# Optimization experiments

Measured on AMD Instinct MI355X. Metric: run time of the kernel, lower is better.

The kernel has to match this reference:

```python
import jax, jax.numpy as jnp
import numpy as np

DEPTH_REF = jnp.array([28.01, 16.32], dtype=jnp.float32)
DIM_REF = jnp.array([[3.88, 1.63, 1.53], [0.84, 1.76, 0.66], [1.78, 1.52, 1.78]], dtype=jnp.float32)
TOPK = 50
DET_THRESHOLD = 0.25
PI = 3.14159265358979


def nms_hm(heat, kernel=3):
    # 3x3 max-pool NMS: keep peaks, zero everything else
    pad = (kernel - 1) // 2
    hmax = jax.lax.reduce_window(heat, -jnp.inf, jax.lax.max,
                                 (1, 1, kernel, kernel), (1, 1, 1, 1),
                                 [(0, 0), (0, 0), (pad, pad), (pad, pad)])
    return jnp.where(hmax == heat, heat, 0.0)


def select_topk(heat, K):
    B, C, H, W = heat.shape
    scores_all, inds_all = jax.lax.top_k(heat.reshape(B, C, H * W), K)  # [B,C,K]
    ys_all = (inds_all // W).astype(jnp.float32)
    xs_all = (inds_all % W).astype(jnp.float32)
    scores, inds = jax.lax.top_k(scores_all.reshape(B, C * K), K)       # [B,K] over classes
    clses = (inds // K).astype(jnp.float32)
    topk_inds = jnp.take_along_axis(inds_all.reshape(B, C * K), inds, axis=1)
    ys = jnp.take_along_axis(ys_all.reshape(B, C * K), inds, axis=1)
    xs = jnp.take_along_axis(xs_all.reshape(B, C * K), inds, axis=1)
    return scores, topk_inds, clses, ys, xs


def select_point_of_interest(index, feature_maps):
    B, Cf, H, W = feature_maps.shape
    fm = feature_maps.transpose(0, 2, 3, 1).reshape(B, H * W, Cf)
    return jnp.take_along_axis(fm, index[:, :, None], axis=1)  # [B,K,Cf]


def encode_box3d(rotys, dims, locs):
    # dims = (l, h, w); corner signs reproduce SMOKE's gather pattern
    N = rotys.shape[0]
    c, s = jnp.cos(rotys), jnp.sin(rotys)
    z, o = jnp.zeros_like(c), jnp.ones_like(c)
    ry = jnp.stack([c, z, s, z, o, z, -s, z, c], axis=1).reshape(N, 3, 3)
    sx = jnp.array([-0.5, 0.5, 0.5, 0.5, 0.5, -0.5, -0.5, -0.5], dtype=dims.dtype)
    sy = jnp.array([-1., -1., 0., 0., -1., -1., 0., 0.], dtype=dims.dtype)
    sz = jnp.array([-0.5, -0.5, -0.5, 0.5, 0.5, 0.5, 0.5, -0.5], dtype=dims.dtype)
    corners = jnp.stack([dims[:, 0:1] * sx, dims[:, 1:2] * sy, dims[:, 2:3] * sz], axis=1)  # [N,3,8]
    return jnp.einsum('nij,njk->nik', ry, corners) + locs[:, :, None]


def setup_inputs() -> dict:
    key = jax.random.key(0)
    k1, k2 = jax.random.split(key)
    B, C, H, W = 32, 3, 192, 640
    IMG_W, IMG_H = 4 * W, 4 * H
    pred_heatmap = jax.random.uniform(k1, (B, C, H, W), dtype=jnp.float32)
    pred_regression = jax.random.normal(k2, (B, 8, H, W), dtype=jnp.float32) * 0.5
    # affine image->heatmap (scale 1/4), invertible
    tm = jnp.array([[0.25, 0., 0.], [0., 0.25, 0.], [0., 0., 1.]], dtype=jnp.float32)
    trans_mat = jnp.tile(tm[None], (B, 1, 1))
    Kc = jnp.array([[721.5, 0., IMG_W / 2.], [0., 721.5, IMG_H / 2.], [0., 0., 1.]], dtype=jnp.float32)
    K_mat = jnp.tile(Kc[None], (B, 1, 1))
    img_size = jnp.tile(jnp.array([[IMG_W, IMG_H]], dtype=jnp.float32), (B, 1))
    return {"pred_heatmap": pred_heatmap, "pred_regression": pred_regression,
            "trans_mat": trans_mat, "K_mat": K_mat, "img_size": img_size}


def reference(pred_heatmap, pred_regression, trans_mat, K_mat, img_size):
    B = pred_heatmap.shape[0]
    heat = nms_hm(pred_heatmap)
    scores, inds, clses, ys, xs = select_topk(heat, TOPK)
    reg = select_point_of_interest(inds, pred_regression).reshape(-1, 8)  # [B*K,8]

    points = jnp.stack([xs.reshape(-1), ys.reshape(-1)], axis=1)          # heatmap coords
    depth_off, proj_off = reg[:, 0], reg[:, 1:3]
    dim_off, ori = reg[:, 3:6], reg[:, 6:8]
    cls_idx = clses.reshape(-1).astype(jnp.int32)

    obj_id = jnp.repeat(jnp.arange(B), TOPK)
    tm_inv = jnp.linalg.inv(trans_mat)[obj_id]   # [N,3,3]
    K_inv = jnp.linalg.inv(K_mat)[obj_id]

    # decode location: heatmap -> image -> camera frame
    proj = points + proj_off
    proj_ext = jnp.concatenate([proj, jnp.ones_like(proj[:, :1])], axis=1)
    proj_img = jnp.einsum('nij,nj->ni', tm_inv, proj_ext)                 # image-plane homog coords
    depths = depth_off * DEPTH_REF[1] + DEPTH_REF[0]
    locs = jnp.einsum('nij,nj->ni', K_inv, proj_img * depths[:, None])

    dims = jnp.exp(dim_off) * DIM_REF[cls_idx]                            # (l,h,w)
    locs = locs.at[:, 1].add(dims[:, 1] / 2)

    # decode orientation
    eps = 1e-7
    rays = jnp.arctan(locs[:, 0] / (locs[:, 2] + eps))
    alphas = jnp.arctan(ori[:, 0] / (ori[:, 1] + eps))
    alphas = jnp.where(ori[:, 1] >= 0, alphas - PI / 2, alphas + PI / 2)
    rotys = alphas + rays
    wrap = lambda a: jnp.where(a > PI, a - 2 * PI, jnp.where(a < -PI, a + 2 * PI, a))
    rotys, alphas = wrap(rotys), wrap(alphas)

    # encode 2D boxes from projected 3D corners
    corners = encode_box3d(rotys, dims, locs)                             # [N,3,8]
    proj2 = jnp.einsum('nij,njk->nik', K_mat[obj_id], corners)
    xy = proj2[:, :2] / proj2[:, 2:3]
    Wi, Hi = img_size[obj_id, 0], img_size[obj_id, 1]
    xmins = jnp.clip(xy[:, 0].min(axis=1), 0.0, Wi)
    ymins = jnp.clip(xy[:, 1].min(axis=1), 0.0, Hi)
    xmaxs = jnp.clip(xy[:, 0].max(axis=1), 0.0, Wi)
    ymaxs = jnp.clip(xy[:, 1].max(axis=1), 0.0, Hi)
    box2d = jnp.stack([xmins, ymins, xmaxs, ymaxs], axis=1)

    dims_rolled = jnp.roll(dims, -1, axis=1)                              # (h,w,l)
    result = jnp.concatenate([
        cls_idx.astype(jnp.float32)[:, None], alphas[:, None], box2d,
        dims_rolled, locs, rotys[:, None], scores.reshape(-1, 1)], axis=1)  # [B*K,14]
    keep = result[:, -1] > DET_THRESHOLD
    return jnp.where(keep[:, None], result, 0.0)
```

## Files before the change

### kernel.cpp

```cpp
#include <hip/hip_runtime.h>
#include <math.h>

#define Hd 192
#define Wd 640
#define HWp (Hd * Wd)
#define NCLS 3
#define KTOP 50
#define NB 32
#define NPL (NB * NCLS)
#define GPR 160
#define GPP (HWp / 4)
#define SPR 40
#define SEGBLK 30
#define SEGCAP 64
#define CAP 2048
#define RBK 256
#define PI_F 3.14159265358979f

#define OFF_COUNTS 0
#define OFF_SEGKEY 16384
#define OFF_PSC 0x200000
#define OFF_PPI 0x206000

__device__ inline float fmax3(float a, float b, float c) {
  return fmaxf(fmaxf(a, b), c);
}

template <typename F>
__device__ inline void peaks_in_group(const float* __restrict__ p, int g, F&& f) {
  const int y = g / GPR;
  const int x0 = (g - y * GPR) * 4;
  const float* rm = p + y * Wd + x0;
  const float4 mq = *(const float4*)rm;
  const float ml = (x0 > 0) ? rm[-1] : -INFINITY;
  const float mr = (x0 + 4 < Wd) ? rm[4] : -INFINITY;
  float4 tq; float tl, tr;
  if (y > 0) {
    const float* rt = rm - Wd;
    tq = *(const float4*)rt;
    tl = (x0 > 0) ? rt[-1] : -INFINITY;
    tr = (x0 + 4 < Wd) ? rt[4] : -INFINITY;
  } else {
    tq.x = tq.y = tq.z = tq.w = -INFINITY; tl = -INFINITY; tr = -INFINITY;
  }
  float4 bq; float bl, br;
  if (y < Hd - 1) {
    const float* rb = rm + Wd;
    bq = *(const float4*)rb;
    bl = (x0 > 0) ? rb[-1] : -INFINITY;
    br = (x0 + 4 < Wd) ? rb[4] : -INFINITY;
  } else {
    bq.x = bq.y = bq.z = bq.w = -INFINITY; bl = -INFINITY; br = -INFINITY;
  }
  const float c0 = fmax3(tl, ml, bl);
  const float c1 = fmax3(tq.x, mq.x, bq.x);
  const float c2 = fmax3(tq.y, mq.y, bq.y);
  const float c3 = fmax3(tq.z, mq.z, bq.z);
  const float c4 = fmax3(tq.w, mq.w, bq.w);
  const float c5 = fmax3(tr, mr, br);
  const int base = y * Wd + x0;
  if (mq.x == fmax3(c0, c1, c2)) f(__float_as_uint(mq.x), base + 0);
  if (mq.y == fmax3(c1, c2, c3)) f(__float_as_uint(mq.y), base + 1);
  if (mq.z == fmax3(c2, c3, c4)) f(__float_as_uint(mq.z), base + 2);
  if (mq.w == fmax3(c3, c4, c5)) f(__float_as_uint(mq.w), base + 3);
}

template <typename F>
__device__ inline void for_each_peak_plane(const float* __restrict__ p, int tid,
                                           int nth, F&& f) {
  for (int g = tid; g < GPP; g += nth) peaks_in_group(p, g, f);
}

__device__ inline unsigned long long mk_key(unsigned int bits, int idx) {
  return ((unsigned long long)bits << 32) | (unsigned int)~idx;
}

__device__ inline int bucket_of(unsigned int bits) {
  const unsigned int base = __float_as_uint(0.995f);
  if (bits <= base) return 0;
  unsigned int d = (bits - base) >> 9;
  return d > 255u ? 255 : (int)d;
}

struct Row16 {
  float4 q0, q1, q2, q3;
  float l, r;
};

__device__ inline Row16 load_row16(const float* __restrict__ rp, int x0, bool valid) {
  Row16 o;
  if (valid) {
    o.q0 = *(const float4*)(rp);
    o.q1 = *(const float4*)(rp + 4);
    o.q2 = *(const float4*)(rp + 8);
    o.q3 = *(const float4*)(rp + 12);
    o.l = (x0 > 0) ? rp[-1] : -INFINITY;
    o.r = (x0 + 16 < Wd) ? rp[16] : -INFINITY;
  } else {
    o.q0.x = o.q0.y = o.q0.z = o.q0.w = -INFINITY;
    o.q1 = o.q0; o.q2 = o.q0; o.q3 = o.q0;
    o.l = -INFINITY; o.r = -INFINITY;
  }
  return o;
}

__device__ inline float4 max3v(const float4 a, const float4 b, const float4 c) {
  float4 o;
  o.x = fmax3(a.x, b.x, c.x);
  o.y = fmax3(a.y, b.y, c.y);
  o.z = fmax3(a.z, b.z, c.z);
  o.w = fmax3(a.w, b.w, c.w);
  return o;
}

__device__ inline void inv3(const float* m, float* o) {
  float a = m[0], b = m[1], c = m[2];
  float d = m[3], e = m[4], f = m[5];
  float g = m[6], h = m[7], i = m[8];
  float A = e * i - f * h;
  float B = -(d * i - f * g);
  float C = d * h - e * g;
  float det = a * A + b * B + c * C;
  float id = 1.0f / det;
  o[0] = A * id;            o[1] = -(b * i - c * h) * id; o[2] = (b * f - c * e) * id;
  o[3] = B * id;            o[4] = (a * i - c * g) * id;  o[5] = -(a * f - c * d) * id;
  o[6] = C * id;            o[7] = -(a * h - b * g) * id; o[8] = (a * e - b * d) * id;
}

__device__ inline float wrap_pi(float a) {
  if (a > PI_F) return a - 2.0f * PI_F;
  if (a < -PI_F) return a + 2.0f * PI_F;
  return a;
}

__constant__ float DIM_REF_C[9] = {3.88f, 1.63f, 1.53f,
                                   0.84f, 1.76f, 0.66f,
                                   1.78f, 1.52f, 1.78f};

__global__ __launch_bounds__(256) void scan_kernel(
    const float* __restrict__ heat,
    int* __restrict__ counts,
    unsigned long long* __restrict__ segkey) {
  const int blk = blockIdx.x;
  const int plane = blk / SEGBLK;
  const int sub = blk - plane * SEGBLK;
  __shared__ unsigned long long s_k[SEGCAP];
  __shared__ int s_n;
  if (threadIdx.x == 0) s_n = 0;
  __syncthreads();

  const int strip = sub * 256 + threadIdx.x;
  const int y = strip / SPR;
  const int x0 = (strip - y * SPR) * 16;
  const float* pm = heat + (size_t)plane * HWp + y * Wd + x0;

  const Row16 m = load_row16(pm, x0, true);
  const Row16 t = load_row16(pm - Wd, x0, y > 0);
  const Row16 b = load_row16(pm + Wd, x0, y < Hd - 1);

  const float cl = fmax3(t.l, m.l, b.l);
  const float cr = fmax3(t.r, m.r, b.r);
  const float4 c0 = max3v(t.q0, m.q0, b.q0);
  const float4 c1 = max3v(t.q1, m.q1, b.q1);
  const float4 c2 = max3v(t.q2, m.q2, b.q2);
  const float4 c3 = max3v(t.q3, m.q3, b.q3);

  const float TH = 0.995f;
  const int base = y * Wd + x0;
#define EMIT(V, W0, W1, W2, J)                                         \
  if ((V) >= TH && (V) == fmax3((W0), (W1), (W2))) {                   \
    int slot = atomicAdd(&s_n, 1);                                     \
    if (slot < SEGCAP) s_k[slot] = mk_key(__float_as_uint(V), base + (J)); \
  }
  EMIT(m.q0.x, cl,   c0.x, c0.y, 0)
  EMIT(m.q0.y, c0.x, c0.y, c0.z, 1)
  EMIT(m.q0.z, c0.y, c0.z, c0.w, 2)
  EMIT(m.q0.w, c0.z, c0.w, c1.x, 3)
  EMIT(m.q1.x, c0.w, c1.x, c1.y, 4)
  EMIT(m.q1.y, c1.x, c1.y, c1.z, 5)
  EMIT(m.q1.z, c1.y, c1.z, c1.w, 6)
  EMIT(m.q1.w, c1.z, c1.w, c2.x, 7)
  EMIT(m.q2.x, c1.w, c2.x, c2.y, 8)
  EMIT(m.q2.y, c2.x, c2.y, c2.z, 9)
  EMIT(m.q2.z, c2.y, c2.z, c2.w, 10)
  EMIT(m.q2.w, c2.z, c2.w, c3.x, 11)
  EMIT(m.q3.x, c2.w, c3.x, c3.y, 12)
  EMIT(m.q3.y, c3.x, c3.y, c3.z, 13)
  EMIT(m.q3.z, c3.y, c3.z, c3.w, 14)
  EMIT(m.q3.w, c3.z, c3.w, cr,   15)
#undef EMIT

  __syncthreads();
  const int n = s_n;
  if (threadIdx.x == 0) counts[blk] = n;
  const int nn = n < SEGCAP ? n : SEGCAP;
  if (threadIdx.x < nn)
    segkey[(size_t)blk * SEGCAP + threadIdx.x] = s_k[threadIdx.x];
}

__global__ __launch_bounds__(256) void rank_kernel(
    const float* __restrict__ heat,
    const int* __restrict__ counts,
    const unsigned long long* __restrict__ segkey,
    float* __restrict__ plane_sc,
    int* __restrict__ plane_pi) {
  const int plane = blockIdx.x;
  const int tid = threadIdx.x;

  __shared__ unsigned long long s_key[CAP];
  __shared__ unsigned long long c_key[CAP];
  __shared__ int s_off[SEGBLK + 1];
  __shared__ int cnt[RBK], suf[RBK], cur[RBK];
  __shared__ int s_flag, s_M, s_fast;
  __shared__ int s_fbB, s_fbAbove, s_fbT, s_fbCnt;

  if (tid == 0) { s_flag = 0; s_off[0] = 0; }
  __syncthreads();
  if (tid < SEGBLK) {
    int nv = counts[plane * SEGBLK + tid];
    if (nv > SEGCAP) { atomicOr(&s_flag, 1); nv = SEGCAP; }
    s_off[tid + 1] = nv;
  }
  __syncthreads();
  if (tid == 0) {
    int acc = 0;
    for (int i = 1; i <= SEGBLK; ++i) { acc += s_off[i]; s_off[i] = acc; }
    s_M = acc;
    s_fast = (s_flag == 0) && (acc >= KTOP) && (acc <= CAP);
  }
  __syncthreads();

  if (s_fast) {
    const unsigned long long* pk = segkey + (size_t)plane * SEGBLK * SEGCAP;
    for (int i = tid; i < SEGBLK * SEGCAP; i += 256) {
      const int sg = i >> 6;
      const int j = i & (SEGCAP - 1);
      const int o = s_off[sg];
      const int nsg = s_off[sg + 1] - o;
      if (j < nsg) s_key[o + j] = pk[i];
    }
    __syncthreads();
  } else {
    const float* hp = heat + (size_t)plane * HWp;
    unsigned int* fb_hist = (unsigned int*)c_key;
    for (int i = tid; i < 1024; i += 256) fb_hist[i] = 0;
    __syncthreads();
    for_each_peak_plane(hp, tid, 256, [&](unsigned int bits, int idx) {
      unsigned int bkt = bits >> 20; if (bkt > 1023u) bkt = 1023u;
      atomicAdd(&fb_hist[bkt], 1u);
    });
    __syncthreads();
    if (tid == 0) {
      int acc = 0, Bs = -1;
      for (int bkt = 1023; bkt >= 0; --bkt) {
        int cc = (int)fb_hist[bkt];
        if (acc + cc >= KTOP) { Bs = bkt; s_fbAbove = acc; break; }
        acc += cc;
      }
      s_fbB = Bs;
      if (Bs < 0) s_fbAbove = acc;
    }
    __syncthreads();
    const int Bs = s_fbB;
    unsigned int T;
    if (Bs < 0) {
      T = 0;
    } else {
      for (int i = tid; i < 1024; i += 256) fb_hist[i] = 0;
      __syncthreads();
      for_each_peak_plane(hp, tid, 256, [&](unsigned int bits, int idx) {
        unsigned int bkt = bits >> 20; if (bkt > 1023u) bkt = 1023u;
        if ((int)bkt == Bs) atomicAdd(&fb_hist[(bits >> 10) & 1023], 1u);
      });
      __syncthreads();
      if (tid == 0) {
        int acc = s_fbAbove, Ss = 0;
        for (int sb = 1023; sb >= 0; --sb) {
          int cc = (int)fb_hist[sb];
          if (acc + cc >= KTOP) { Ss = sb; break; }
          acc += cc;
        }
        s_fbT = (int)(((unsigned int)Bs << 20) | ((unsigned int)Ss << 10));
      }
      __syncthreads();
      T = (unsigned int)s_fbT;
    }
    if (tid == 0) s_fbCnt = 0;
    __syncthreads();
    for_each_peak_plane(hp, tid, 256, [&](unsigned int bits, int idx) {
      if (bits >= T) {
        int slot = atomicAdd(&s_fbCnt, 1);
        if (slot < CAP) s_key[slot] = mk_key(bits, idx);
      }
    });
    __syncthreads();
    if (tid == 0) s_M = s_fbCnt < CAP ? s_fbCnt : CAP;
    __syncthreads();
  }
  const int M = s_M;

  cnt[tid] = 0;
  cur[tid] = 0;
  __syncthreads();
  for (int i = tid; i < M; i += 256)
    atomicAdd(&cnt[bucket_of((unsigned int)(s_key[i] >> 32))], 1);
  __syncthreads();
  suf[tid] = cnt[tid];
  __syncthreads();
#pragma unroll
  for (int d = 1; d < RBK; d <<= 1) {
    const int v = (tid + d < RBK) ? suf[tid + d] : 0;
    __syncthreads();
    suf[tid] += v;
    __syncthreads();
  }
  {
    const int excl = suf[tid] - cnt[tid];
    __syncthreads();
    suf[tid] = excl;
  }
  __syncthreads();
  for (int i = tid; i < M; i += 256) {
    const unsigned long long k = s_key[i];
    const int bq = bucket_of((unsigned int)(k >> 32));
    const int slot = suf[bq] + atomicAdd(&cur[bq], 1);
    c_key[slot] = k;
  }
  __syncthreads();
  float* psc = plane_sc + plane * 64;
  int* ppi = plane_pi + plane * 64;
  for (int i = tid; i < M; i += 256) {
    const unsigned long long k = c_key[i];
    const int bq = bucket_of((unsigned int)(k >> 32));
    const int st = suf[bq];
    const int nb = cnt[bq];
    int rank = st;
    for (int tt = st; tt < st + nb; ++tt) rank += (c_key[tt] > k);
    if (rank < KTOP) {
      psc[rank] = __uint_as_float((unsigned int)(k >> 32));
      ppi[rank] = (int)~((unsigned int)k);
    }
  }
  for (int s2 = M + tid; s2 < KTOP; s2 += 256) {
    psc[s2] = 0.0f;
    ppi[s2] = 0;
  }
}

__global__ __launch_bounds__(256) void decode_kernel(
    const float* __restrict__ plane_sc,
    const int* __restrict__ plane_pi,
    const float* __restrict__ regr,
    const float* __restrict__ trans_mat,
    const float* __restrict__ K_mat,
    const float* __restrict__ img_size,
    float* __restrict__ out) {
  const int b = blockIdx.x;
  const int tid = threadIdx.x;

  __shared__ float d_sc[NCLS * KTOP];
  __shared__ int d_pi[NCLS * KTOP];
  __shared__ int sel[KTOP];

  if (tid < NCLS * KTOP) {
    const int c = tid / KTOP;
    const int k2 = tid - c * KTOP;
    d_sc[tid] = plane_sc[(b * NCLS + c) * 64 + k2];
    d_pi[tid] = plane_pi[(b * NCLS + c) * 64 + k2];
  }
  __syncthreads();

  if (tid < NCLS * KTOP) {
    const float v = d_sc[tid];
    int rank = 0;
    for (int j = 0; j < NCLS * KTOP; ++j) {
      const float w = d_sc[j];
      rank += (w > v) || (w == v && j < tid);
    }
    if (rank < KTOP) sel[rank] = tid;
  }
  __syncthreads();

  if (tid < KTOP) {
    const int i = sel[tid];
    const int cls = i / KTOP;
    const float score = d_sc[i];
    const int ind = d_pi[i];
    const float ys = (float)(ind / Wd);
    const float xs = (float)(ind - (ind / Wd) * Wd);

    const float* rb = regr + (size_t)b * 8 * HWp + ind;
    const float r0 = rb[0 * HWp], r1 = rb[1 * HWp], r2 = rb[2 * HWp], r3 = rb[3 * HWp];
    const float r4 = rb[4 * HWp], r5 = rb[5 * HWp], r6 = rb[6 * HWp], r7 = rb[7 * HWp];

    float tm[9], km[9], tmi[9], kmi[9];
#pragma unroll
    for (int q = 0; q < 9; ++q) { tm[q] = trans_mat[b * 9 + q]; km[q] = K_mat[b * 9 + q]; }
    inv3(tm, tmi);
    inv3(km, kmi);

    const float px = xs + r1, py = ys + r2;
    const float gx = tmi[0] * px + tmi[1] * py + tmi[2];
    const float gy = tmi[3] * px + tmi[4] * py + tmi[5];
    const float gz = tmi[6] * px + tmi[7] * py + tmi[8];
    const float depth = r0 * 16.32f + 28.01f;
    const float qx = gx * depth, qy = gy * depth, qz = gz * depth;
    const float lx = kmi[0] * qx + kmi[1] * qy + kmi[2] * qz;
    float ly = kmi[3] * qx + kmi[4] * qy + kmi[5] * qz;
    const float lz = kmi[6] * qx + kmi[7] * qy + kmi[8] * qz;

    const float d0 = expf(r3) * DIM_REF_C[cls * 3 + 0];
    const float d1 = expf(r4) * DIM_REF_C[cls * 3 + 1];
    const float d2 = expf(r5) * DIM_REF_C[cls * 3 + 2];
    ly += d1 * 0.5f;

    const float ray = atanf(lx / (lz + 1e-7f));
    float alpha = atanf(r6 / (r7 + 1e-7f));
    alpha += (r7 >= 0.0f) ? -PI_F * 0.5f : PI_F * 0.5f;
    const float roty = wrap_pi(alpha + ray);
    alpha = wrap_pi(alpha);

    const float SX[8] = {-0.5f, 0.5f, 0.5f, 0.5f, 0.5f, -0.5f, -0.5f, -0.5f};
    const float SY[8] = {-1.0f, -1.0f, 0.0f, 0.0f, -1.0f, -1.0f, 0.0f, 0.0f};
    const float SZ[8] = {-0.5f, -0.5f, -0.5f, 0.5f, 0.5f, 0.5f, 0.5f, -0.5f};
    const float cr = cosf(roty), sr = sinf(roty);
    float minx = INFINITY, maxx = -INFINITY, miny = INFINITY, maxy = -INFINITY;
#pragma unroll
    for (int j = 0; j < 8; ++j) {
      const float ax = d0 * SX[j], ay = d1 * SY[j], az = d2 * SZ[j];
      const float cx = cr * ax + sr * az + lx;
      const float cy = ay + ly;
      const float cz = -sr * ax + cr * az + lz;
      const float ppx = km[0] * cx + km[1] * cy + km[2] * cz;
      const float ppy = km[3] * cx + km[4] * cy + km[5] * cz;
      const float ppz = km[6] * cx + km[7] * cy + km[8] * cz;
      const float X = ppx / ppz, Y = ppy / ppz;
      minx = fminf(minx, X); maxx = fmaxf(maxx, X);
      miny = fminf(miny, Y); maxy = fmaxf(maxy, Y);
    }
    const float Wi = img_size[b * 2 + 0], Hi = img_size[b * 2 + 1];
    const float xmin = fminf(fmaxf(minx, 0.0f), Wi);
    const float ymin = fminf(fmaxf(miny, 0.0f), Hi);
    const float xmax = fminf(fmaxf(maxx, 0.0f), Wi);
    const float ymax = fminf(fmaxf(maxy, 0.0f), Hi);

    float* o = out + (size_t)(b * KTOP + tid) * 14;
    if (score > 0.25f) {
      o[0] = (float)cls; o[1] = alpha;
      o[2] = xmin; o[3] = ymin; o[4] = xmax; o[5] = ymax;
      o[6] = d1; o[7] = d2; o[8] = d0;
      o[9] = lx; o[10] = ly; o[11] = lz;
      o[12] = roty; o[13] = score;
    } else {
#pragma unroll
      for (int q = 0; q < 14; ++q) o[q] = 0.0f;
    }
  }
}


extern "C" void kernel_launch(void* const* d_in, const int* in_sizes, int n_in,
                              void* d_out, int out_size, void* d_ws, size_t ws_size,
                              hipStream_t stream) {
  const float* heat = (const float*)d_in[0];
  const float* regr = (const float*)d_in[1];
  const float* tmat = (const float*)d_in[2];
  const float* kmat = (const float*)d_in[3];
  const float* isz = (const float*)d_in[4];

  char* ws = (char*)d_ws;
  int* counts = (int*)(ws + OFF_COUNTS);
  unsigned long long* segkey = (unsigned long long*)(ws + OFF_SEGKEY);
  float* plane_sc = (float*)(ws + OFF_PSC);
  int* plane_pi = (int*)(ws + OFF_PPI);

  scan_kernel<<<NPL * SEGBLK, 256, 0, stream>>>(heat, counts, segkey);
  rank_kernel<<<NPL, 256, 0, stream>>>(heat, counts, segkey,
                                       plane_sc, plane_pi);
  decode_kernel<<<NB, 256, 0, stream>>>(plane_sc, plane_pi,
                                        regr, tmat, kmat, isz,
                                        (float*)d_out);
}
```

Baseline: 211.5 us.

## Fuse peak scan with per-segment top-K and merge segments in decode

Merges the scan and rank kernels into one kernel, so each of 576 blocks scans a sixth of a heatmap plane and computes its local top-50, with an in-block histogram threshold fallback when candidates overflow. The decode kernel then merges the six segment lists per class using 64-bit packed keys and a bucket prefilter, and falls back to a full-plane scan only when a class has fewer than K candidates. This drops one kernel launch and the global round trip of segment keys. In exchange each block does more serial work and uses more shared memory, and the decode kernel grows larger.

```diff
diff --git a/kernel.cpp b/kernel.cpp
--- a/kernel.cpp
+++ b/kernel.cpp
@@ -8,78 +8,42 @@
 #define KTOP 50
 #define NB 32
 #define NPL (NB * NCLS)
+#define SPR 40
+#define TSTR (Hd * SPR)
+#define NSUB 6
+#define SSTR (TSTR / NSUB)
+#define CAPS 512
+#define CAP 2048
+#define RBK 256
 #define GPR 160
 #define GPP (HWp / 4)
-#define SPR 40
-#define SEGBLK 30
-#define SEGCAP 64
-#define CAP 2048
-#define RBK 256
+#define NMERGE (NCLS * NSUB * KTOP)
+#define TH_F 0.995f
 #define PI_F 3.14159265358979f
 
-#define OFF_COUNTS 0
-#define OFF_SEGKEY 16384
-#define OFF_PSC 0x200000
-#define OFF_PPI 0x206000
+#define OFF_SSC 0
+#define OFF_SPI 0x40000
+#define OFF_SCNT 0x80000
 
 __device__ inline float fmax3(float a, float b, float c) {
   return fmaxf(fmaxf(a, b), c);
 }
 
-template <typename F>
-__device__ inline void peaks_in_group(const float* __restrict__ p, int g, F&& f) {
-  const int y = g / GPR;
-  const int x0 = (g - y * GPR) * 4;
-  const float* rm = p + y * Wd + x0;
-  const float4 mq = *(const float4*)rm;
-  const float ml = (x0 > 0) ? rm[-1] : -INFINITY;
-  const float mr = (x0 + 4 < Wd) ? rm[4] : -INFINITY;
-  float4 tq; float tl, tr;
-  if (y > 0) {
-    const float* rt = rm - Wd;
-    tq = *(const float4*)rt;
-    tl = (x0 > 0) ? rt[-1] : -INFINITY;
-    tr = (x0 + 4 < Wd) ? rt[4] : -INFINITY;
-  } else {
-    tq.x = tq.y = tq.z = tq.w = -INFINITY; tl = -INFINITY; tr = -INFINITY;
-  }
-  float4 bq; float bl, br;
-  if (y < Hd - 1) {
-    const float* rb = rm + Wd;
-    bq = *(const float4*)rb;
-    bl = (x0 > 0) ? rb[-1] : -INFINITY;
-    br = (x0 + 4 < Wd) ? rb[4] : -INFINITY;
-  } else {
-    bq.x = bq.y = bq.z = bq.w = -INFINITY; bl = -INFINITY; br = -INFINITY;
-  }
-  const float c0 = fmax3(tl, ml, bl);
-  const float c1 = fmax3(tq.x, mq.x, bq.x);
-  const float c2 = fmax3(tq.y, mq.y, bq.y);
-  const float c3 = fmax3(tq.z, mq.z, bq.z);
-  const float c4 = fmax3(tq.w, mq.w, bq.w);
-  const float c5 = fmax3(tr, mr, br);
-  const int base = y * Wd + x0;
-  if (mq.x == fmax3(c0, c1, c2)) f(__float_as_uint(mq.x), base + 0);
-  if (mq.y == fmax3(c1, c2, c3)) f(__float_as_uint(mq.y), base + 1);
-  if (mq.z == fmax3(c2, c3, c4)) f(__float_as_uint(mq.z), base + 2);
-  if (mq.w == fmax3(c3, c4, c5)) f(__float_as_uint(mq.w), base + 3);
-}
-
-template <typename F>
-__device__ inline void for_each_peak_plane(const float* __restrict__ p, int tid,
-                                           int nth, F&& f) {
-  for (int g = tid; g < GPP; g += nth) peaks_in_group(p, g, f);
-}
-
 __device__ inline unsigned long long mk_key(unsigned int bits, int idx) {
   return ((unsigned long long)bits << 32) | (unsigned int)~idx;
 }
 
 __device__ inline int bucket_of(unsigned int bits) {
-  const unsigned int base = __float_as_uint(0.995f);
+  const unsigned int base = __float_as_uint(TH_F);
   if (bits <= base) return 0;
   unsigned int d = (bits - base) >> 9;
   return d > 255u ? 255 : (int)d;
+}
+
+__device__ inline unsigned long long mk_key19(unsigned int bits, int cls, int idx) {
+  return ((unsigned long long)bits << 19) |
+         ((unsigned long long)(2 - cls) << 17) |
+         (unsigned long long)((idx ^ 0x1FFFF) & 0x1FFFF);
 }
 
 struct Row16 {
@@ -113,65 +77,24 @@
   return o;
 }
 
-__device__ inline void inv3(const float* m, float* o) {
-  float a = m[0], b = m[1], c = m[2];
-  float d = m[3], e = m[4], f = m[5];
-  float g = m[6], h = m[7], i = m[8];
-  float A = e * i - f * h;
-  float B = -(d * i - f * g);
-  float C = d * h - e * g;
-  float det = a * A + b * B + c * C;
-  float id = 1.0f / det;
-  o[0] = A * id;            o[1] = -(b * i - c * h) * id; o[2] = (b * f - c * e) * id;
-  o[3] = B * id;            o[4] = (a * i - c * g) * id;  o[5] = -(a * f - c * d) * id;
-  o[6] = C * id;            o[7] = -(a * h - b * g) * id; o[8] = (a * e - b * d) * id;
-}
-
-__device__ inline float wrap_pi(float a) {
-  if (a > PI_F) return a - 2.0f * PI_F;
-  if (a < -PI_F) return a + 2.0f * PI_F;
-  return a;
-}
-
-__constant__ float DIM_REF_C[9] = {3.88f, 1.63f, 1.53f,
-                                   0.84f, 1.76f, 0.66f,
-                                   1.78f, 1.52f, 1.78f};
-
-__global__ __launch_bounds__(256) void scan_kernel(
-    const float* __restrict__ heat,
-    int* __restrict__ counts,
-    unsigned long long* __restrict__ segkey) {
-  const int blk = blockIdx.x;
-  const int plane = blk / SEGBLK;
-  const int sub = blk - plane * SEGBLK;
-  __shared__ unsigned long long s_k[SEGCAP];
-  __shared__ int s_n;
-  if (threadIdx.x == 0) s_n = 0;
-  __syncthreads();
-
-  const int strip = sub * 256 + threadIdx.x;
+template <typename F>
+__device__ inline void strip_peaks(const float* __restrict__ hp, int strip, F&& f) {
   const int y = strip / SPR;
   const int x0 = (strip - y * SPR) * 16;
-  const float* pm = heat + (size_t)plane * HWp + y * Wd + x0;
-
+  const float* pm = hp + y * Wd + x0;
   const Row16 m = load_row16(pm, x0, true);
   const Row16 t = load_row16(pm - Wd, x0, y > 0);
   const Row16 b = load_row16(pm + Wd, x0, y < Hd - 1);
-
   const float cl = fmax3(t.l, m.l, b.l);
   const float cr = fmax3(t.r, m.r, b.r);
   const float4 c0 = max3v(t.q0, m.q0, b.q0);
   const float4 c1 = max3v(t.q1, m.q1, b.q1);
   const float4 c2 = max3v(t.q2, m.q2, b.q2);
   const float4 c3 = max3v(t.q3, m.q3, b.q3);
-
-  const float TH = 0.995f;
   const int base = y * Wd + x0;
-#define EMIT(V, W0, W1, W2, J)                                         \
-  if ((V) >= TH && (V) == fmax3((W0), (W1), (W2))) {                   \
-    int slot = atomicAdd(&s_n, 1);                                     \
-    if (slot < SEGCAP) s_k[slot] = mk_key(__float_as_uint(V), base + (J)); \
-  }
+#define EMIT(V, W0, W1, W2, J)                                       \
+  if ((V) >= TH_F && (V) == fmax3((W0), (W1), (W2)))                 \
+    f(__float_as_uint(V), base + (J));
   EMIT(m.q0.x, cl,   c0.x, c0.y, 0)
   EMIT(m.q0.y, c0.x, c0.y, c0.z, 1)
   EMIT(m.q0.z, c0.y, c0.z, c0.w, 2)
@@ -189,120 +112,169 @@
   EMIT(m.q3.z, c3.y, c3.z, c3.w, 14)
   EMIT(m.q3.w, c3.z, c3.w, cr,   15)
 #undef EMIT
-
-  __syncthreads();
-  const int n = s_n;
-  if (threadIdx.x == 0) counts[blk] = n;
-  const int nn = n < SEGCAP ? n : SEGCAP;
-  if (threadIdx.x < nn)
-    segkey[(size_t)blk * SEGCAP + threadIdx.x] = s_k[threadIdx.x];
-}
-
-__global__ __launch_bounds__(256) void rank_kernel(
+}
+
+template <typename F>
+__device__ inline void peaks_in_group(const float* __restrict__ p, int g, F&& f) {
+  const int y = g / GPR;
+  const int x0 = (g - y * GPR) * 4;
+  const float* rm = p + y * Wd + x0;
+  const float4 mq = *(const float4*)rm;
+  const float ml = (x0 > 0) ? rm[-1] : -INFINITY;
+  const float mr = (x0 + 4 < Wd) ? rm[4] : -INFINITY;
+  float4 tq; float tl, tr;
+  if (y > 0) {
+    const float* rt = rm - Wd;
+    tq = *(const float4*)rt;
+    tl = (x0 > 0) ? rt[-1] : -INFINITY;
+    tr = (x0 + 4 < Wd) ? rt[4] : -INFINITY;
+  } else {
+    tq.x = tq.y = tq.z = tq.w = -INFINITY; tl = -INFINITY; tr = -INFINITY;
+  }
+  float4 bq; float bl, br;
+  if (y < Hd - 1) {
+    const float* rb = rm + Wd;
+    bq = *(const float4*)rb;
+    bl = (x0 > 0) ? rb[-1] : -INFINITY;
+    br = (x0 + 4 < Wd) ? rb[4] : -INFINITY;
+  } else {
+    bq.x = bq.y = bq.z = bq.w = -INFINITY; bl = -INFINITY; br = -INFINITY;
+  }
+  const float c0 = fmax3(tl, ml, bl);
+  const float c1 = fmax3(tq.x, mq.x, bq.x);
+  const float c2 = fmax3(tq.y, mq.y, bq.y);
+  const float c3 = fmax3(tq.z, mq.z, bq.z);
+  const float c4 = fmax3(tq.w, mq.w, bq.w);
+  const float c5 = fmax3(tr, mr, br);
+  const int base = y * Wd + x0;
+  if (mq.x == fmax3(c0, c1, c2)) f(__float_as_uint(mq.x), base + 0);
+  if (mq.y == fmax3(c1, c2, c3)) f(__float_as_uint(mq.y), base + 1);
+  if (mq.z == fmax3(c2, c3, c4)) f(__float_as_uint(mq.z), base + 2);
+  if (mq.w == fmax3(c3, c4, c5)) f(__float_as_uint(mq.w), base + 3);
+}
+
+template <typename F>
+__device__ inline void for_each_peak_plane(const float* __restrict__ p, int tid,
+                                           int nth, F&& f) {
+  for (int g = tid; g < GPP; g += nth) peaks_in_group(p, g, f);
+}
+
+__device__ inline void inv3(const float* m, float* o) {
+  float a = m[0], b = m[1], c = m[2];
+  float d = m[3], e = m[4], f = m[5];
+  float g = m[6], h = m[7], i = m[8];
+  float A = e * i - f * h;
+  float B = -(d * i - f * g);
+  float C = d * h - e * g;
+  float det = a * A + b * B + c * C;
+  float id = 1.0f / det;
+  o[0] = A * id;            o[1] = -(b * i - c * h) * id; o[2] = (b * f - c * e) * id;
+  o[3] = B * id;            o[4] = (a * i - c * g) * id;  o[5] = -(a * f - c * d) * id;
+  o[6] = C * id;            o[7] = -(a * h - b * g) * id; o[8] = (a * e - b * d) * id;
+}
+
+__device__ inline float wrap_pi(float a) {
+  if (a > PI_F) return a - 2.0f * PI_F;
+  if (a < -PI_F) return a + 2.0f * PI_F;
+  return a;
+}
+
+__constant__ float DIM_REF_C[9] = {3.88f, 1.63f, 1.53f,
+                                   0.84f, 1.76f, 0.66f,
+                                   1.78f, 1.52f, 1.78f};
+
+__global__ __launch_bounds__(256) void scanrank_kernel(
     const float* __restrict__ heat,
-    const int* __restrict__ counts,
-    const unsigned long long* __restrict__ segkey,
-    float* __restrict__ plane_sc,
-    int* __restrict__ plane_pi) {
-  const int plane = blockIdx.x;
+    float* __restrict__ ssc,
+    int* __restrict__ spi,
+    int* __restrict__ scnt) {
+  const int blk = blockIdx.x;
   const int tid = threadIdx.x;
-
-  __shared__ unsigned long long s_key[CAP];
-  __shared__ unsigned long long c_key[CAP];
-  __shared__ int s_off[SEGBLK + 1];
+  const int plane = blk / NSUB;
+  const int sub = blk - plane * NSUB;
+  const float* hp = heat + (size_t)plane * HWp;
+  const int sbase = sub * SSTR;
+
+  __shared__ unsigned long long s_key[CAPS];
+  __shared__ unsigned long long c_key[CAPS];
   __shared__ int cnt[RBK], suf[RBK], cur[RBK];
-  __shared__ int s_flag, s_M, s_fast;
-  __shared__ int s_fbB, s_fbAbove, s_fbT, s_fbCnt;
-
-  if (tid == 0) { s_flag = 0; s_off[0] = 0; }
-  __syncthreads();
-  if (tid < SEGBLK) {
-    int nv = counts[plane * SEGBLK + tid];
-    if (nv > SEGCAP) { atomicOr(&s_flag, 1); nv = SEGCAP; }
-    s_off[tid + 1] = nv;
-  }
-  __syncthreads();
-  if (tid == 0) {
-    int acc = 0;
-    for (int i = 1; i <= SEGBLK; ++i) { acc += s_off[i]; s_off[i] = acc; }
-    s_M = acc;
-    s_fast = (s_flag == 0) && (acc >= KTOP) && (acc <= CAP);
-  }
-  __syncthreads();
-
-  if (s_fast) {
-    const unsigned long long* pk = segkey + (size_t)plane * SEGBLK * SEGCAP;
-    for (int i = tid; i < SEGBLK * SEGCAP; i += 256) {
-      const int sg = i >> 6;
-      const int j = i & (SEGCAP - 1);
-      const int o = s_off[sg];
-      const int nsg = s_off[sg + 1] - o;
-      if (j < nsg) s_key[o + j] = pk[i];
-    }
-    __syncthreads();
-  } else {
-    const float* hp = heat + (size_t)plane * HWp;
-    unsigned int* fb_hist = (unsigned int*)c_key;
-    for (int i = tid; i < 1024; i += 256) fb_hist[i] = 0;
-    __syncthreads();
-    for_each_peak_plane(hp, tid, 256, [&](unsigned int bits, int idx) {
-      unsigned int bkt = bits >> 20; if (bkt > 1023u) bkt = 1023u;
-      atomicAdd(&fb_hist[bkt], 1u);
+  __shared__ int s_n, s_B, s_above, s_T;
+
+  if (tid == 0) s_n = 0;
+  __syncthreads();
+
+  for (int it = 0; it < SSTR / 256; ++it) {
+    const int strip = sbase + it * 256 + tid;
+    strip_peaks(hp, strip, [&](unsigned int bits, int idx) {
+      int slot = atomicAdd(&s_n, 1);
+      if (slot < CAPS) s_key[slot] = mk_key(bits, idx);
     });
+  }
+  __syncthreads();
+  int n = s_n;
+
+  if (n > CAPS) {
+    unsigned int* hist = (unsigned int*)c_key;
+    const unsigned int THB = __float_as_uint(TH_F);
+    for (int i = tid; i < 1024; i += 256) hist[i] = 0;
+    __syncthreads();
+    for (int it = 0; it < SSTR / 256; ++it) {
+      const int strip = sbase + it * 256 + tid;
+      strip_peaks(hp, strip, [&](unsigned int bits, int idx) {
+        atomicAdd(&hist[(bits - THB) >> 7], 1u);
+      });
+    }
     __syncthreads();
     if (tid == 0) {
-      int acc = 0, Bs = -1;
-      for (int bkt = 1023; bkt >= 0; --bkt) {
-        int cc = (int)fb_hist[bkt];
-        if (acc + cc >= KTOP) { Bs = bkt; s_fbAbove = acc; break; }
+      int acc = 0, res = 0, above = 0;
+      for (int q = 655; q >= 0; --q) {
+        int cc = (int)hist[q];
+        if (acc + cc >= KTOP) { res = q; above = acc; break; }
         acc += cc;
       }
-      s_fbB = Bs;
-      if (Bs < 0) s_fbAbove = acc;
-    }
-    __syncthreads();
-    const int Bs = s_fbB;
-    unsigned int T;
-    if (Bs < 0) {
-      T = 0;
-    } else {
-      for (int i = tid; i < 1024; i += 256) fb_hist[i] = 0;
-      __syncthreads();
-      for_each_peak_plane(hp, tid, 256, [&](unsigned int bits, int idx) {
-        unsigned int bkt = bits >> 20; if (bkt > 1023u) bkt = 1023u;
-        if ((int)bkt == Bs) atomicAdd(&fb_hist[(bits >> 10) & 1023], 1u);
+      s_B = res; s_above = above;
+    }
+    __syncthreads();
+    const int Bc = s_B;
+    for (int i = tid; i < 1024; i += 256) hist[i] = 0;
+    __syncthreads();
+    for (int it = 0; it < SSTR / 256; ++it) {
+      const int strip = sbase + it * 256 + tid;
+      strip_peaks(hp, strip, [&](unsigned int bits, int idx) {
+        if ((int)((bits - THB) >> 7) == Bc)
+          atomicAdd(&hist[(bits - THB) & 127], 1u);
       });
-      __syncthreads();
-      if (tid == 0) {
-        int acc = s_fbAbove, Ss = 0;
-        for (int sb = 1023; sb >= 0; --sb) {
-          int cc = (int)fb_hist[sb];
-          if (acc + cc >= KTOP) { Ss = sb; break; }
-          acc += cc;
+    }
+    __syncthreads();
+    if (tid == 0) {
+      int acc = s_above, S = 0;
+      for (int sb = 127; sb >= 0; --sb) {
+        int cc = (int)hist[sb];
+        if (acc + cc >= KTOP) { S = sb; break; }
+        acc += cc;
+      }
+      s_T = (int)(THB + ((unsigned int)Bc << 7) + (unsigned int)S);
+      s_n = 0;
+    }
+    __syncthreads();
+    const unsigned int T = (unsigned int)s_T;
+    for (int it = 0; it < SSTR / 256; ++it) {
+      const int strip = sbase + it * 256 + tid;
+      strip_peaks(hp, strip, [&](unsigned int bits, int idx) {
+        if (bits >= T) {
+          int slot = atomicAdd(&s_n, 1);
+          if (slot < CAPS) s_key[slot] = mk_key(bits, idx);
         }
-        s_fbT = (int)(((unsigned int)Bs << 20) | ((unsigned int)Ss << 10));
-      }
-      __syncthreads();
-      T = (unsigned int)s_fbT;
-    }
-    if (tid == 0) s_fbCnt = 0;
-    __syncthreads();
-    for_each_peak_plane(hp, tid, 256, [&](unsigned int bits, int idx) {
-      if (bits >= T) {
-        int slot = atomicAdd(&s_fbCnt, 1);
-        if (slot < CAP) s_key[slot] = mk_key(bits, idx);
-      }
-    });
-    __syncthreads();
-    if (tid == 0) s_M = s_fbCnt < CAP ? s_fbCnt : CAP;
-    __syncthreads();
-  }
-  const int M = s_M;
+      });
+    }
+    __syncthreads();
+    n = s_n < CAPS ? s_n : CAPS;
+  }
 
   cnt[tid] = 0;
   cur[tid] = 0;
   __syncthreads();
-  for (int i = tid; i < M; i += 256)
+  for (int i = tid; i < n; i += 256)
     atomicAdd(&cnt[bucket_of((unsigned int)(s_key[i] >> 32))], 1);
   __syncthreads();
   suf[tid] = cnt[tid];
@@ -320,16 +292,16 @@
     suf[tid] = excl;
   }
   __syncthreads();
-  for (int i = tid; i < M; i += 256) {
+  for (int i = tid; i < n; i += 256) {
     const unsigned long long k = s_key[i];
     const int bq = bucket_of((unsigned int)(k >> 32));
     const int slot = suf[bq] + atomicAdd(&cur[bq], 1);
     c_key[slot] = k;
   }
   __syncthreads();
-  float* psc = plane_sc + plane * 64;
-  int* ppi = plane_pi + plane * 64;
-  for (int i = tid; i < M; i += 256) {
+  float* psc = ssc + blk * 64;
+  int* ppi = spi + blk * 64;
+  for (int i = tid; i < n; i += 256) {
     const unsigned long long k = c_key[i];
     const int bq = bucket_of((unsigned int)(k >> 32));
     const int st = suf[bq];
@@ -341,15 +313,18 @@
       ppi[rank] = (int)~((unsigned int)k);
     }
   }
-  for (int s2 = M + tid; s2 < KTOP; s2 += 256) {
+  for (int s2 = n + tid; s2 < KTOP; s2 += 256) {
     psc[s2] = 0.0f;
     ppi[s2] = 0;
   }
+  if (tid == 0) scnt[blk] = n;
 }
 
 __global__ __launch_bounds__(256) void decode_kernel(
-    const float* __restrict__ plane_sc,
-    const int* __restrict__ plane_pi,
+    const float* __restrict__ heat,
+    const float* __restrict__ ssc,
+    const int* __restrict__ spi,
+    const int* __restrict__ scnt,
     const float* __restrict__ regr,
     const float* __restrict__ trans_mat,
     const float* __restrict__ K_mat,
@@ -358,34 +333,190 @@
   const int b = blockIdx.x;
   const int tid = threadIdx.x;
 
-  __shared__ float d_sc[NCLS * KTOP];
-  __shared__ int d_pi[NCLS * KTOP];
+  __shared__ unsigned long long d_keys[NMERGE];
+  __shared__ unsigned long long f_keys[NCLS * KTOP];
+  __shared__ unsigned char d_in[NMERGE];
+  __shared__ int hb[NCLS][RBK];
+  __shared__ int s_bq[NCLS];
+  __shared__ int s_ct[NCLS];
   __shared__ int sel[KTOP];
+  __shared__ unsigned long long s_key[CAP];
+  __shared__ unsigned long long c_key[CAP];
+  __shared__ int cnt[RBK], suf[RBK], cur[RBK];
+  __shared__ int s_fbB, s_fbAbove, s_fbT, s_fbCnt;
+
+  if (tid < NCLS) {
+    int t = 0;
+    for (int s = 0; s < NSUB; ++s) t += scnt[(b * NCLS + tid) * NSUB + s];
+    s_ct[tid] = t;
+  }
+  __syncthreads();
+
+  for (int i = tid; i < NMERGE; i += 256) {
+    const int c = i / (NSUB * KTOP);
+    const int rem = i - c * (NSUB * KTOP);
+    const int s = rem / KTOP;
+    const int k2 = rem - s * KTOP;
+    const int sb = (b * NCLS + c) * NSUB + s;
+    const float v = ssc[sb * 64 + k2];
+    const int idx = spi[sb * 64 + k2];
+    d_keys[i] = mk_key19(__float_as_uint(v), c, idx);
+  }
+  __syncthreads();
+
+  for (int c = 0; c < NCLS; ++c) {
+    if (s_ct[c] < KTOP) {
+      const float* hp = heat + (size_t)(b * NCLS + c) * HWp;
+      unsigned int* fb_hist = (unsigned int*)c_key;
+      for (int i = tid; i < 1024; i += 256) fb_hist[i] = 0;
+      __syncthreads();
+      for_each_peak_plane(hp, tid, 256, [&](unsigned int bits, int idx) {
+        unsigned int bkt = bits >> 20; if (bkt > 1023u) bkt = 1023u;
+        atomicAdd(&fb_hist[bkt], 1u);
+      });
+      __syncthreads();
+      if (tid == 0) {
+        int acc = 0, Bs = -1;
+        for (int bkt = 1023; bkt >= 0; --bkt) {
+          int cc = (int)fb_hist[bkt];
+          if (acc + cc >= KTOP) { Bs = bkt; s_fbAbove = acc; break; }
+          acc += cc;
+        }
+        s_fbB = Bs;
+        if (Bs < 0) s_fbAbove = acc;
+      }
+      __syncthreads();
+      const int Bs = s_fbB;
+      unsigned int T;
+      if (Bs < 0) {
+        T = 0;
+      } else {
+        for (int i = tid; i < 1024; i += 256) fb_hist[i] = 0;
+        __syncthreads();
+        for_each_peak_plane(hp, tid, 256, [&](unsigned int bits, int idx) {
+          unsigned int bkt = bits >> 20; if (bkt > 1023u) bkt = 1023u;
+          if ((int)bkt == Bs) atomicAdd(&fb_hist[(bits >> 10) & 1023], 1u);
+        });
+        __syncthreads();
+        if (tid == 0) {
+          int acc = s_fbAbove, Ss = 0;
+          for (int sb = 1023; sb >= 0; --sb) {
+            int cc = (int)fb_hist[sb];
+            if (acc + cc >= KTOP) { Ss = sb; break; }
+            acc += cc;
+          }
+          s_fbT = (int)(((unsigned int)Bs << 20) | ((unsigned int)Ss << 10));
+        }
+        __syncthreads();
+        T = (unsigned int)s_fbT;
+      }
+      if (tid == 0) s_fbCnt = 0;
+      __syncthreads();
+      for_each_peak_plane(hp, tid, 256, [&](unsigned int bits, int idx) {
+        if (bits >= T) {
+          int slot = atomicAdd(&s_fbCnt, 1);
+          if (slot < CAP) s_key[slot] = mk_key(bits, idx);
+        }
+      });
+      __syncthreads();
+      const int M = s_fbCnt < CAP ? s_fbCnt : CAP;
+      cnt[tid] = 0; cur[tid] = 0;
+      __syncthreads();
+      for (int i = tid; i < M; i += 256)
+        atomicAdd(&cnt[bucket_of((unsigned int)(s_key[i] >> 32))], 1);
+      __syncthreads();
+      suf[tid] = cnt[tid];
+      __syncthreads();
+#pragma unroll
+      for (int d = 1; d < RBK; d <<= 1) {
+        const int v = (tid + d < RBK) ? suf[tid + d] : 0;
+        __syncthreads();
+        suf[tid] += v;
+        __syncthreads();
+      }
+      {
+        const int excl = suf[tid] - cnt[tid];
+        __syncthreads();
+        suf[tid] = excl;
+      }
+      __syncthreads();
+      for (int i = tid; i < M; i += 256) {
+        const unsigned long long k = s_key[i];
+        const int bq = bucket_of((unsigned int)(k >> 32));
+        const int slot = suf[bq] + atomicAdd(&cur[bq], 1);
+        c_key[slot] = k;
+      }
+      __syncthreads();
+      for (int i = tid; i < NMERGE / NCLS; i += 256)
+        d_keys[c * (NSUB * KTOP) + i] = mk_key19(0u, c, 0);
+      __syncthreads();
+      for (int i = tid; i < M; i += 256) {
+        const unsigned long long k = c_key[i];
+        const int bq = bucket_of((unsigned int)(k >> 32));
+        const int st = suf[bq];
+        const int nb = cnt[bq];
+        int rank = st;
+        for (int tt = st; tt < st + nb; ++tt) rank += (c_key[tt] > k);
+        if (rank < KTOP)
+          d_keys[c * (NSUB * KTOP) + rank] =
+              mk_key19((unsigned int)(k >> 32), c, (int)~((unsigned int)k));
+      }
+      __syncthreads();
+    }
+  }
+
+  for (int i = tid; i < NCLS * RBK; i += 256) ((int*)hb)[i] = 0;
+  __syncthreads();
+  for (int i = tid; i < NMERGE; i += 256) {
+    const int c = i / (NSUB * KTOP);
+    atomicAdd(&hb[c][bucket_of((unsigned int)(d_keys[i] >> 19))], 1);
+  }
+  __syncthreads();
+  if (tid < NCLS) {
+    int acc = 0, res = 0;
+    for (int q = RBK - 1; q >= 0; --q) {
+      acc += hb[tid][q];
+      if (acc >= KTOP) { res = q; break; }
+    }
+    s_bq[tid] = res;
+  }
+  __syncthreads();
+  for (int i = tid; i < NMERGE; i += 256) {
+    const int c = i / (NSUB * KTOP);
+    d_in[i] = bucket_of((unsigned int)(d_keys[i] >> 19)) >= s_bq[c];
+  }
+  __syncthreads();
+  for (int i = tid; i < NMERGE; i += 256) {
+    if (!d_in[i]) continue;
+    const int c = i / (NSUB * KTOP);
+    const int lo = c * (NSUB * KTOP), hi = lo + (NSUB * KTOP);
+    const unsigned long long k = d_keys[i];
+    int rank = 0;
+    for (int j = lo; j < hi; ++j) {
+      if (!d_in[j]) continue;
+      const unsigned long long w = d_keys[j];
+      rank += (w > k) || (w == k && j < i);
+    }
+    if (rank < KTOP) f_keys[c * KTOP + rank] = k;
+  }
+  __syncthreads();
 
   if (tid < NCLS * KTOP) {
-    const int c = tid / KTOP;
-    const int k2 = tid - c * KTOP;
-    d_sc[tid] = plane_sc[(b * NCLS + c) * 64 + k2];
-    d_pi[tid] = plane_pi[(b * NCLS + c) * 64 + k2];
-  }
-  __syncthreads();
-
-  if (tid < NCLS * KTOP) {
-    const float v = d_sc[tid];
+    const unsigned long long k = f_keys[tid];
     int rank = 0;
     for (int j = 0; j < NCLS * KTOP; ++j) {
-      const float w = d_sc[j];
-      rank += (w > v) || (w == v && j < tid);
+      const unsigned long long w = f_keys[j];
+      rank += (w > k) || (w == k && j < tid);
     }
     if (rank < KTOP) sel[rank] = tid;
   }
   __syncthreads();
 
   if (tid < KTOP) {
-    const int i = sel[tid];
-    const int cls = i / KTOP;
-    const float score = d_sc[i];
-    const int ind = d_pi[i];
+    const unsigned long long k = f_keys[sel[tid]];
+    const float score = __uint_as_float((unsigned int)(k >> 19));
+    const int cls = 2 - (int)((k >> 17) & 3);
+    const int ind = ((int)(k & 0x1FFFF)) ^ 0x1FFFF;
     const float ys = (float)(ind / Wd);
     const float xs = (float)(ind - (ind / Wd) * Wd);
 
@@ -469,15 +600,12 @@
   const float* isz = (const float*)d_in[4];
 
   char* ws = (char*)d_ws;
-  int* counts = (int*)(ws + OFF_COUNTS);
-  unsigned long long* segkey = (unsigned long long*)(ws + OFF_SEGKEY);
-  float* plane_sc = (float*)(ws + OFF_PSC);
-  int* plane_pi = (int*)(ws + OFF_PPI);
-
-  scan_kernel<<<NPL * SEGBLK, 256, 0, stream>>>(heat, counts, segkey);
-  rank_kernel<<<NPL, 256, 0, stream>>>(heat, counts, segkey,
-                                       plane_sc, plane_pi);
-  decode_kernel<<<NB, 256, 0, stream>>>(plane_sc, plane_pi,
+  float* ssc = (float*)(ws + OFF_SSC);
+  int* spi = (int*)(ws + OFF_SPI);
+  int* scnt = (int*)(ws + OFF_SCNT);
+
+  scanrank_kernel<<<NPL * NSUB, 256, 0, stream>>>(heat, ssc, spi, scnt);
+  decode_kernel<<<NB, 256, 0, stream>>>(heat, ssc, spi, scnt,
                                         regr, tmat, kmat, isz,
                                         (float*)d_out);
 }
```

New measurement: 284.0 us. +34.3%, slower.
